# Performance work log

Measured on AMD Instinct MI355X. Metric: run time of the kernel, lower is better.

## Reference

```python
import jax, jax.numpy as jnp
import numpy as np

EPS = 1e-5

def _inst_norm(x):
    # x: (B,C,H,W); torch .var(dim=2) is unbiased (ddof=1) over HW
    B, C, H, W = x.shape
    xf = x.reshape(B, C, H * W)
    mean = xf.mean(axis=2, keepdims=True)
    var = xf.var(axis=2, ddof=1, keepdims=True) + EPS
    return ((xf - mean) / jnp.sqrt(var)).reshape(B, C, H, W)

def _conv1x1(x, w, b):
    # (out,in) weight applied channelwise
    return jnp.einsum('oc,bchw->bohw', w, x) + b[None, :, None, None]

def setup_inputs() -> dict:
    key = jax.random.key(0)
    ks = jax.random.split(key, 10)
    B, C, H, W = 4, 512, 64, 64
    s = 1.0 / np.sqrt(C)
    return {
        'x_fcc': jax.random.normal(ks[0], (B, C, H, W), jnp.float32),
        'x_fss': jax.random.normal(ks[1], (B, C, H, W), jnp.float32),
        'w1': jax.random.normal(ks[2], (C, C), jnp.float32) * s,
        'b1': jax.random.normal(ks[3], (C,), jnp.float32) * 0.01,
        'w2': jax.random.normal(ks[4], (C, C), jnp.float32) * s,
        'b2': jax.random.normal(ks[5], (C,), jnp.float32) * 0.01,
        'w3': jax.random.normal(ks[6], (C, C), jnp.float32) * s,
        'b3': jax.random.normal(ks[7], (C,), jnp.float32) * 0.01,
        'wrs': jax.random.normal(ks[8], (C, C), jnp.float32) * s,
        'brs': jax.random.normal(ks[9], (C,), jnp.float32) * 0.01,
    }

def reference(x_fcc, x_fss, w1, b1, w2, b2, w3, b3, wrs, brs):
    Bc, Cc, Hc, Wc = x_fcc.shape
    Bs, Cs, Hs, Ws = x_fss.shape
    q = _conv1x1(_inst_norm(x_fcc), w1, b1).reshape(Bc, Cc, Hc * Wc)
    k = _conv1x1(_inst_norm(x_fss), w2, b2).reshape(Bs, Cs, Hs * Ws)
    v = _conv1x1(x_fss, w3, b3).reshape(Bc, Cs, Hs * Ws)
    # attention: (B, HWc, HWs), softmax over style positions
    scores = jnp.einsum('bcq,bck->bqk', q, k)
    A = jax.nn.softmax(scores, axis=-1)
    # aggregate style values per content position: (B, C, HWc)
    frs = jnp.einsum('bck,bqk->bcq', v, A).reshape(x_fcc.shape)
    frs = _conv1x1(frs, wrs, brs)
    return frs + x_fcc
```

## Files before the change

kernel.cpp:

```cpp
#include <hip/hip_runtime.h>
#include <hip/hip_bf16.h>


typedef _Float16 f16_t;
typedef _Float16 f16x8 __attribute__((ext_vector_type(8)));
typedef float f32x4 __attribute__((ext_vector_type(4)));

#define C_DIM 512
#define HW_DIM 4096
#define NBATCH 4
#define CHW (512L * 4096L)

__device__ inline f32x4 mfma_f16(f16x8 a, f16x8 b, f32x4 c) {
    return __builtin_amdgcn_mfma_f32_16x16x32_f16(a, b, c, 0, 0, 0);
}

__device__ inline void g2l16(const f16_t* g, f16_t* l) {
    auto gp = (const __attribute__((address_space(1))) uint32_t*)(uintptr_t)g;
    auto lp = (__attribute__((address_space(3))) uint32_t*)(uint32_t)(uintptr_t)l;
    __builtin_amdgcn_global_load_lds(gp, lp, 16, 0, 0);
}

template<int N> __device__ inline void vmwait() {
    static_assert(N == 0 || N == 2, "add vmcnt case");
    if constexpr (N == 0) asm volatile("s_waitcnt vmcnt(0)" ::: "memory");
    else                  asm volatile("s_waitcnt vmcnt(2)" ::: "memory");
}

__device__ inline void barrier_mem() {
    asm volatile("s_barrier" ::: "memory");
    __builtin_amdgcn_sched_barrier(0);
}

__global__ __launch_bounds__(256) void stats_kernel(
    const float* __restrict__ xc, const float* __restrict__ xs,
    float* __restrict__ meanc, float* __restrict__ rstdc,
    float* __restrict__ means, float* __restrict__ rstds)
{
    int id = blockIdx.x;
    int bc = id & 2047;
    const float4* x = (const float4*)((id < 2048 ? xc : xs) + (size_t)bc * HW_DIM);
    int tid = threadIdx.x;
    float s = 0.f, ss = 0.f;
#pragma unroll
    for (int i = 0; i < 4; i++) {
        float4 v = x[tid + (i << 8)];
        s += v.x + v.y + v.z + v.w;
        ss += v.x * v.x + v.y * v.y + v.z * v.z + v.w * v.w;
    }
#pragma unroll
    for (int o = 32; o; o >>= 1) { s += __shfl_down(s, o); ss += __shfl_down(ss, o); }
    __shared__ float red[8];
    if ((tid & 63) == 0) { red[(tid >> 6) * 2] = s; red[(tid >> 6) * 2 + 1] = ss; }
    __syncthreads();
    if (tid == 0) {
        s  = red[0] + red[2] + red[4] + red[6];
        ss = red[1] + red[3] + red[5] + red[7];
        float mean = s * (1.0f / 4096.0f);
        float var  = (ss - 4096.0f * mean * mean) * (1.0f / 4095.0f);
        float rstd = rsqrtf(var + 1e-5f);
        if (id < 2048) { meanc[bc] = mean; rstdc[bc] = rstd; }
        else           { means[bc] = mean; rstds[bc] = rstd; }
    }
}

__global__ __launch_bounds__(256) void pack_w4_kernel(
    const float* __restrict__ w0, const float* __restrict__ w1,
    const float* __restrict__ w2, const float* __restrict__ w3,
    f16_t* __restrict__ h0, f16_t* __restrict__ h1,
    f16_t* __restrict__ h2, f16_t* __restrict__ h3,
    const float* __restrict__ bb0, const float* __restrict__ bb1,
    const float* __restrict__ bb2, const float* __restrict__ bb3,
    float* __restrict__ biasws)
{
    int which = blockIdx.y;
    const float* w = which == 0 ? w0 : which == 1 ? w1 : which == 2 ? w2 : w3;
    f16_t* h = which == 0 ? h0 : which == 1 ? h1 : which == 2 ? h2 : h3;
    const float* bs = which == 0 ? bb0 : which == 1 ? bb1 : which == 2 ? bb2 : bb3;
    int i = blockIdx.x * 256 + threadIdx.x;
    h[i] = (f16_t)w[i];
    if (i < C_DIM) biasws[which * C_DIM + i] = bs[i];
}

__global__ __launch_bounds__(256) void pack_T_kernel(
    const float* __restrict__ xc, const float* __restrict__ xs,
    const float* __restrict__ meanc, const float* __restrict__ rstdc,
    const float* __restrict__ means, const float* __restrict__ rstds,
    f16_t* __restrict__ ch, f16_t* __restrict__ sh, f16_t* __restrict__ sraw)
{
    __shared__ float tile[32][33];
    int z = blockIdx.z;
    int b = z & 3, src = z >> 2;
    const float* x    = (src == 0) ? xc : xs;
    const float* mean = (src == 0) ? meanc : means;
    const float* rstd = (src == 0) ? rstdc : rstds;

    int c0 = blockIdx.y * 32, p0 = blockIdx.x * 32;
    int tp = threadIdx.x & 31, tc8 = threadIdx.x >> 5;
    const float* xb = x + ((size_t)b * C_DIM + c0) * HW_DIM + p0;
#pragma unroll
    for (int it = 0; it < 4; it++) {
        int c = tc8 + it * 8;
        tile[c][tp] = xb[(size_t)c * HW_DIM + tp];
    }
    __syncthreads();
    int wc = threadIdx.x & 31, wp8 = threadIdx.x >> 5;
    float m = mean[b * C_DIM + c0 + wc];
    float r = rstd[b * C_DIM + c0 + wc];
    size_t obase = ((size_t)b * HW_DIM + p0) * C_DIM + c0;
    f16_t* ohb = ((src == 0) ? ch : sh) + obase;
    f16_t* srb = sraw + obase;
#pragma unroll
    for (int it = 0; it < 4; it++) {
        int p = wp8 + it * 8;
        float v = tile[wc][p];
        ohb[(size_t)p * C_DIM + wc] = (f16_t)((v - m) * r);
        if (src == 1) srb[(size_t)p * C_DIM + wc] = (f16_t)v;
    }
}

__global__ __launch_bounds__(256) void softmax_rows(
    const float* __restrict__ S, f16_t* __restrict__ P)
{
    int row = blockIdx.x;
    int tid = threadIdx.x;
    int wave = tid >> 6, lane = tid & 63;
    const float4* sr = (const float4*)(S + (size_t)row * HW_DIM);
    float4 v[4];
    float mx = -3.4e38f;
#pragma unroll
    for (int i = 0; i < 4; i++) {
        v[i] = sr[tid + (i << 8)];
        mx = fmaxf(mx, fmaxf(fmaxf(v[i].x, v[i].y), fmaxf(v[i].z, v[i].w)));
    }
#pragma unroll
    for (int o = 32; o; o >>= 1) mx = fmaxf(mx, __shfl_down(mx, o));
    __shared__ float red[4];
    if (lane == 0) red[wave] = mx;
    __syncthreads();
    mx = fmaxf(fmaxf(red[0], red[1]), fmaxf(red[2], red[3]));
    float sum = 0.f;
#pragma unroll
    for (int i = 0; i < 4; i++) {
        v[i].x = __expf(v[i].x - mx); v[i].y = __expf(v[i].y - mx);
        v[i].z = __expf(v[i].z - mx); v[i].w = __expf(v[i].w - mx);
        sum += v[i].x + v[i].y + v[i].z + v[i].w;
    }
#pragma unroll
    for (int o = 32; o; o >>= 1) sum += __shfl_down(sum, o);
    __syncthreads();
    if (lane == 0) red[wave] = sum;
    __syncthreads();
    sum = red[0] + red[1] + red[2] + red[3];
    float inv = 1.0f / sum;
    uint2* pr = (uint2*)(P + (size_t)row * HW_DIM);
#pragma unroll
    for (int i = 0; i < 4; i++) {
        union { uint2 u; f16_t h[4]; } o;
        o.h[0] = (f16_t)(v[i].x * inv); o.h[1] = (f16_t)(v[i].y * inv);
        o.h[2] = (f16_t)(v[i].z * inv); o.h[3] = (f16_t)(v[i].w * inv);
        pr[tid + (i << 8)] = o.u;
    }
}

__global__ __launch_bounds__(256) void reduce4_kernel(
    const float* __restrict__ part, f16_t* __restrict__ out)
{
    size_t i = (size_t)blockIdx.x * 256 + threadIdx.x;
    const float4* p0 = (const float4*)part;
    const float4* p1 = (const float4*)(part + CHW);
    const float4* p2 = (const float4*)(part + 2 * CHW);
    const float4* p3 = (const float4*)(part + 3 * CHW);
    float4 a = p0[i], b = p1[i], c = p2[i], d = p3[i];
    union { uint2 u; f16_t h[4]; } o;
    o.h[0] = (f16_t)(a.x + b.x + c.x + d.x);
    o.h[1] = (f16_t)(a.y + b.y + c.y + d.y);
    o.h[2] = (f16_t)(a.z + b.z + c.z + d.z);
    o.h[3] = (f16_t)(a.w + b.w + c.w + d.w);
    ((uint2*)out)[i] = o.u;
}

template<int EPI, bool QK, int NT, int CHX, int CHY>
__global__ __launch_bounds__(512, 2) void gemm256(
    const f16_t* __restrict__ Ah, const f16_t* __restrict__ Bh,
    void* __restrict__ Cout0, const float* __restrict__ bias,
    const float* __restrict__ resid,
    int lda, int ldc,
    long sAz, long sBz, long sCz, long sRz, long sAw, long sBw, long sCw)
{
    constexpr int UNIT = 128 * 64;
    __shared__ __align__(16) f16_t smem[8 * UNIT];

    int bx, by, bz;
    {
        const int nbx = gridDim.x, nby = gridDim.y, nbz = gridDim.z;
        const int lin = ((int)blockIdx.z * nby + blockIdx.y) * nbx + blockIdx.x;
        const int nwg = nbx * nby * nbz;
        const int cpx = nwg >> 3;
        const int logical = (lin & 7) * cpx + (lin >> 3);
        constexpr int CHB = CHX * CHY;
        const int chunk  = logical / CHB;
        const int within = logical % CHB;
        const int cx = within % CHX, cy = within / CHX;
        const int chunks_x = nbx / CHX;
        const int chx = chunk % chunks_x;
        int tt = chunk / chunks_x;
        const int chunks_y = nby / CHY;
        bz = tt / chunks_y;
        by = (tt % chunks_y) * CHY + cy;
        bx = chx * CHX + cx;
    }

    const int tid  = threadIdx.x;
    const int wave = tid >> 6, lane = tid & 63;
    const int wm = (wave >> 2) * 128;
    const int wn = (wave & 3) * 64;
    const int fr = lane & 15;
    const int g16 = lane >> 4;
    const int key = fr & 7;
    const int ha  = wave >> 2;
    const int hb  = wn >> 7;
    const int rB  = wn - hb * 128;

    const int z   = QK ? (bz & 3) : bz;
    const int sel = QK ? (bz >> 2) : 0;
    const f16_t* Az = Ah + (size_t)z * sAz + (size_t)sel * sAw;
    const f16_t* Bz = Bh + (size_t)z * sBz + (size_t)sel * sBw;
    const float* biasp = bias ? (bias + (QK ? sel * C_DIM : 0)) : nullptr;
    const long mBlock = (long)by * 256;
    const long nBlock = (long)bx * 256;

    const int srow8 = lane >> 3;
    const int gsrc  = ((lane & 7) ^ srow8) * 8;
    const f16_t* aRow[2][2]; const f16_t* bRow[2][2];
#pragma unroll
    for (int h = 0; h < 2; h++)
#pragma unroll
        for (int q = 0; q < 2; q++) {
            long r = q * 64 + wave * 8 + srow8;
            aRow[h][q] = Az + (size_t)(mBlock + h * 128 + r) * lda + gsrc;
            bRow[h][q] = Bz + (size_t)(nBlock + h * 128 + r) * lda + gsrc;
        }
    const int dst0 = wave * 512;
    const int dst1 = 4096 + wave * 512;

    auto stageU = [&](int t, int isB, int h) {
        f16_t* ub = smem + ((t & 1) * 4 + isB * 2 + h) * UNIT;
        const long k0 = (long)t * 64;
        if (isB) {
            g2l16(bRow[h][0] + k0, ub + dst0);
            g2l16(bRow[h][1] + k0, ub + dst1);
        } else {
            g2l16(aRow[h][0] + k0, ub + dst0);
            g2l16(aRow[h][1] + k0, ub + dst1);
        }
    };

    f32x4 acc[8][4];
#pragma unroll
    for (int i = 0; i < 8; i++)
#pragma unroll
        for (int j = 0; j < 4; j++) acc[i][j] = (f32x4){0.f, 0.f, 0.f, 0.f};

    stageU(0, 0, 0); stageU(0, 0, 1); stageU(0, 1, 0); stageU(0, 1, 1);
    if (NT > 1) stageU(1, 0, 0);
    vmwait<2>();
    barrier_mem();

#pragma unroll
    for (int t = 0; t < NT; ++t) {
        const f16_t* bufA = smem + ((t & 1) * 4 + ha) * UNIT;
        const f16_t* bufB = smem + ((t & 1) * 4 + 2 + hb) * UNIT;
#pragma unroll
        for (int ks = 0; ks < 2; ++ks) {
            const int gr = ((ks * 4 + g16) ^ key) * 8;
            f16x8 a[8], b0, b1;
#pragma unroll
            for (int mi = 0; mi < 8; mi++)
                a[mi] = *reinterpret_cast<const f16x8*>(
                    bufA + (mi * 16 + fr) * 64 + gr);
            b0 = *reinterpret_cast<const f16x8*>(bufB + (rB + fr) * 64 + gr);
            b1 = *reinterpret_cast<const f16x8*>(bufB + (rB + 16 + fr) * 64 + gr);
            if (ks == 0) { if (t + 1 < NT) stageU(t + 1, 0, 1); }
            else         { if (t + 1 < NT) stageU(t + 1, 1, 1); }
            barrier_mem();
            __builtin_amdgcn_s_setprio(1);
#pragma unroll
            for (int mi = 0; mi < 8; mi++) {
                acc[mi][0] = mfma_f16(a[mi], b0, acc[mi][0]);
                acc[mi][1] = mfma_f16(a[mi], b1, acc[mi][1]);
            }
            __builtin_amdgcn_s_setprio(0);
            barrier_mem();
            b0 = *reinterpret_cast<const f16x8*>(bufB + (rB + 32 + fr) * 64 + gr);
            b1 = *reinterpret_cast<const f16x8*>(bufB + (rB + 48 + fr) * 64 + gr);
            if (ks == 0) { if (t + 1 < NT) stageU(t + 1, 1, 0); }
            else {
                if (t + 2 < NT) { stageU(t + 2, 0, 0); vmwait<2>(); }
                else if (t + 1 < NT) vmwait<0>();
            }
            barrier_mem();
            __builtin_amdgcn_s_setprio(1);
#pragma unroll
            for (int mi = 0; mi < 8; mi++) {
                acc[mi][2] = mfma_f16(a[mi], b0, acc[mi][2]);
                acc[mi][3] = mfma_f16(a[mi], b1, acc[mi][3]);
            }
            __builtin_amdgcn_s_setprio(0);
            barrier_mem();
        }
    }

    const int col  = lane & 15;
    const int rowq = (lane >> 4) * 4;
    const size_t cbase = (size_t)z * sCz + (size_t)sel * sCw;
#pragma unroll
    for (int mi = 0; mi < 8; mi++) {
        const long mb = mBlock + wm + mi * 16 + rowq;
        float bv[4];
#pragma unroll
        for (int r = 0; r < 4; r++) bv[r] = biasp ? biasp[mb + r] : 0.0f;
#pragma unroll
        for (int j2 = 0; j2 < 4; j2++) {
            const long n = nBlock + wn + j2 * 16 + col;
            float v[4];
#pragma unroll
            for (int r = 0; r < 4; r++) v[r] = acc[mi][j2][r] + bv[r];
            if constexpr (EPI == 0) {
                float* O = (float*)Cout0 + cbase;
                const float* R = resid ? (resid + (size_t)z * sRz) : nullptr;
#pragma unroll
                for (int r = 0; r < 4; r++) {
                    size_t off = (size_t)(mb + r) * ldc + n;
                    O[off] = v[r] + (R ? R[off] : 0.0f);
                }
            } else if constexpr (EPI == 1) {
                f16_t* O = (f16_t*)Cout0 + cbase;
#pragma unroll
                for (int r = 0; r < 4; r++) O[(size_t)(mb + r) * ldc + n] = (f16_t)v[r];
            } else if constexpr (EPI == 3) {
                alignas(8) f16_t h[4];
#pragma unroll
                for (int r = 0; r < 4; r++) h[r] = (f16_t)v[r];
                *reinterpret_cast<uint2*>((f16_t*)Cout0 + cbase + (size_t)n * ldc + mb)
                    = *reinterpret_cast<uint2*>(h);
            } else {
                alignas(16) float h[4];
#pragma unroll
                for (int r = 0; r < 4; r++) h[r] = v[r];
                *reinterpret_cast<float4*>((float*)Cout0 + cbase + (size_t)n * ldc + mb)
                    = *reinterpret_cast<float4*>(h);
            }
        }
    }
}

extern "C" void kernel_launch(void* const* d_in, const int* in_sizes, int n_in,
                              void* d_out, int out_size, void* d_ws, size_t ws_size,
                              hipStream_t stream)
{
    const float* x_fcc = (const float*)d_in[0];
    const float* x_fss = (const float*)d_in[1];
    const float* w1 = (const float*)d_in[2];
    const float* b1 = (const float*)d_in[3];
    const float* w2 = (const float*)d_in[4];
    const float* b2 = (const float*)d_in[5];
    const float* w3 = (const float*)d_in[6];
    const float* b3 = (const float*)d_in[7];
    const float* wrs = (const float*)d_in[8];
    const float* brs = (const float*)d_in[9];
    float* out = (float*)d_out;
    (void)n_in; (void)in_sizes; (void)out_size; (void)ws_size;

    char* base = (char*)d_ws;
    size_t off = 0;
    auto take = [&](size_t bytes) -> char* {
        char* p = base + off;
        off += (bytes + 255) & ~(size_t)255;
        return p;
    };
    const size_t WB = (size_t)C_DIM * C_DIM * sizeof(f16_t);
    const size_t TB = (size_t)NBATCH * CHW * sizeof(f16_t);
    const long  TBe = NBATCH * CHW;

    float* meanc = (float*)take(2048 * 4);
    float* rstdc = (float*)take(2048 * 4);
    float* means = (float*)take(2048 * 4);
    float* rstds = (float*)take(2048 * 4);
    float* biasws = (float*)take(4 * C_DIM * 4);
    f16_t* w1h = (f16_t*)take(WB);
    f16_t* w2h = (f16_t*)take(WB);
    f16_t* w3h = (f16_t*)take(WB);
    f16_t* wrh = (f16_t*)take(WB);
    f16_t* qT = (f16_t*)take(TB);
    f16_t* kT = (f16_t*)take(TB);
    f16_t* vh   = (f16_t*)take(TB);
    f16_t* frsT = (f16_t*)take(TB);
    char* packb = take(8 * TB);
    f16_t* xcT  = (f16_t*)(packb);
    f16_t* xsT  = (f16_t*)(packb + TB);
    f16_t* xsrT = (f16_t*)(packb + 2 * TB);
    float* Smat = (float*)(packb);
    f16_t* Pmat = (f16_t*)(packb + 4 * TB);
    float* Part = (float*)(packb + 6 * TB);

    dim3 blk(256);
    dim3 blk5(512);

    stats_kernel<<<dim3(4096), blk, 0, stream>>>(x_fcc, x_fss, meanc, rstdc, means, rstds);
    pack_w4_kernel<<<dim3(1024, 4), blk, 0, stream>>>(
        w1, w2, w3, wrs, w1h, w2h, w3h, wrh, b1, b2, b3, brs, biasws);
    pack_T_kernel<<<dim3(128, 16, 8), blk, 0, stream>>>(
        x_fcc, x_fss, meanc, rstdc, means, rstds, xcT, xsT, xsrT);
    gemm256<3, true, 8, 8, 2><<<dim3(16, 2, 8), blk5, 0, stream>>>(
        w1h, xcT, qT, biasws, nullptr, C_DIM, C_DIM,
        0L, CHW, CHW, 0L, (long)C_DIM * C_DIM, TBe, TBe);
    gemm256<1, false, 8, 8, 2><<<dim3(16, 2, 4), blk5, 0, stream>>>(
        w3h, xsrT, vh, biasws + 2 * C_DIM, nullptr, C_DIM, HW_DIM,
        0L, CHW, CHW, 0L, 0L, 0L, 0L);
    for (int b = 0; b < NBATCH; b++) {
        gemm256<0, false, 8, 4, 8><<<dim3(16, 16, 1), blk5, 0, stream>>>(
            qT + (size_t)b * CHW, kT + (size_t)b * CHW,
            Smat, nullptr, nullptr, C_DIM, HW_DIM,
            0L, 0L, 0L, 0L, 0L, 0L, 0L);
        softmax_rows<<<dim3(4096), blk, 0, stream>>>(Smat, Pmat);
        gemm256<4, false, 16, 8, 2><<<dim3(16, 2, 4), blk5, 0, stream>>>(
            vh + (size_t)b * CHW, Pmat,
            Part, nullptr, nullptr, HW_DIM, C_DIM,
            1024L, 1024L, CHW, 0L, 0L, 0L, 0L);
        reduce4_kernel<<<dim3(CHW / 1024), blk, 0, stream>>>(
            Part, frsT + (size_t)b * CHW);
    }
    gemm256<0, false, 8, 8, 2><<<dim3(16, 2, 4), blk5, 0, stream>>>(
        wrh, frsT, out, biasws + 3 * C_DIM, x_fcc, C_DIM, HW_DIM,
        0L, CHW, CHW, CHW, 0L, 0L, 0L);
}
```

Before: 599.5 us.

## Add 256x128 triple-buffered GEMM and deepen prefetch in 256x256 GEMM

Adds a new gemm128r kernel with a 256x128 tile and a three-stage LDS ring buffer. It is used for the V projection, the P·V partial GEMMs and the output projection, which doubles their workgroup count so more CUs get work. The existing 256x256 kernel is renamed and its prefetch schedule is reordered to issue a whole K-tile ahead, with the vmcnt waits moved after the MFMAs. The triple buffer uses more LDS per block (about 144KB), which may limit occupancy, and the smaller N tile lowers data reuse per block.

```diff
diff --git a/kernel.cpp b/kernel.cpp
--- a/kernel.cpp
+++ b/kernel.cpp
@@ -22,14 +22,36 @@
 }
 
 template<int N> __device__ inline void vmwait() {
-    static_assert(N == 0 || N == 2, "add vmcnt case");
-    if constexpr (N == 0) asm volatile("s_waitcnt vmcnt(0)" ::: "memory");
-    else                  asm volatile("s_waitcnt vmcnt(2)" ::: "memory");
+    static_assert(N == 0 || N == 2 || N == 4 || N == 6, "add vmcnt case");
+    if constexpr (N == 0)      asm volatile("s_waitcnt vmcnt(0)" ::: "memory");
+    else if constexpr (N == 2) asm volatile("s_waitcnt vmcnt(2)" ::: "memory");
+    else if constexpr (N == 4) asm volatile("s_waitcnt vmcnt(4)" ::: "memory");
+    else                       asm volatile("s_waitcnt vmcnt(6)" ::: "memory");
 }
 
 __device__ inline void barrier_mem() {
     asm volatile("s_barrier" ::: "memory");
     __builtin_amdgcn_sched_barrier(0);
+}
+
+template<int CHX, int CHY>
+__device__ inline void xcd_swizzle(int& bx, int& by, int& bz) {
+    const int nbx = gridDim.x, nby = gridDim.y, nbz = gridDim.z;
+    const int lin = ((int)blockIdx.z * nby + blockIdx.y) * nbx + blockIdx.x;
+    const int nwg = nbx * nby * nbz;
+    const int cpx = nwg >> 3;
+    const int logical = (lin & 7) * cpx + (lin >> 3);
+    constexpr int CHB = CHX * CHY;
+    const int chunk  = logical / CHB;
+    const int within = logical % CHB;
+    const int cx = within % CHX, cy = within / CHX;
+    const int chunks_x = nbx / CHX;
+    const int chx = chunk % chunks_x;
+    int tt = chunk / chunks_x;
+    const int chunks_y = nby / CHY;
+    bz = tt / chunks_y;
+    by = (tt % chunks_y) * CHY + cy;
+    bx = chx * CHX + cx;
 }
 
 __global__ __launch_bounds__(256) void stats_kernel(
@@ -181,7 +203,7 @@
 }
 
 template<int EPI, bool QK, int NT, int CHX, int CHY>
-__global__ __launch_bounds__(512, 2) void gemm256(
+__global__ __launch_bounds__(512, 2) void gemm256d(
     const f16_t* __restrict__ Ah, const f16_t* __restrict__ Bh,
     void* __restrict__ Cout0, const float* __restrict__ bias,
     const float* __restrict__ resid,
@@ -192,24 +214,7 @@
     __shared__ __align__(16) f16_t smem[8 * UNIT];
 
     int bx, by, bz;
-    {
-        const int nbx = gridDim.x, nby = gridDim.y, nbz = gridDim.z;
-        const int lin = ((int)blockIdx.z * nby + blockIdx.y) * nbx + blockIdx.x;
-        const int nwg = nbx * nby * nbz;
-        const int cpx = nwg >> 3;
-        const int logical = (lin & 7) * cpx + (lin >> 3);
-        constexpr int CHB = CHX * CHY;
-        const int chunk  = logical / CHB;
-        const int within = logical % CHB;
-        const int cx = within % CHX, cy = within / CHX;
-        const int chunks_x = nbx / CHX;
-        const int chx = chunk % chunks_x;
-        int tt = chunk / chunks_x;
-        const int chunks_y = nby / CHY;
-        bz = tt / chunks_y;
-        by = (tt % chunks_y) * CHY + cy;
-        bx = chx * CHX + cx;
-    }
+    xcd_swizzle<CHX, CHY>(bx, by, bz);
 
     const int tid  = threadIdx.x;
     const int wave = tid >> 6, lane = tid & 63;
@@ -263,8 +268,8 @@
         for (int j = 0; j < 4; j++) acc[i][j] = (f32x4){0.f, 0.f, 0.f, 0.f};
 
     stageU(0, 0, 0); stageU(0, 0, 1); stageU(0, 1, 0); stageU(0, 1, 1);
-    if (NT > 1) stageU(1, 0, 0);
-    vmwait<2>();
+    if (NT > 1) { stageU(1, 0, 0); stageU(1, 0, 1); }
+    vmwait<4>();
     barrier_mem();
 
 #pragma unroll
@@ -281,8 +286,7 @@
                     bufA + (mi * 16 + fr) * 64 + gr);
             b0 = *reinterpret_cast<const f16x8*>(bufB + (rB + fr) * 64 + gr);
             b1 = *reinterpret_cast<const f16x8*>(bufB + (rB + 16 + fr) * 64 + gr);
-            if (ks == 0) { if (t + 1 < NT) stageU(t + 1, 0, 1); }
-            else         { if (t + 1 < NT) stageU(t + 1, 1, 1); }
+            if (ks == 0 && t + 1 < NT) stageU(t + 1, 1, 0);
             barrier_mem();
             __builtin_amdgcn_s_setprio(1);
 #pragma unroll
@@ -294,10 +298,10 @@
             barrier_mem();
             b0 = *reinterpret_cast<const f16x8*>(bufB + (rB + 32 + fr) * 64 + gr);
             b1 = *reinterpret_cast<const f16x8*>(bufB + (rB + 48 + fr) * 64 + gr);
-            if (ks == 0) { if (t + 1 < NT) stageU(t + 1, 1, 0); }
-            else {
-                if (t + 2 < NT) { stageU(t + 2, 0, 0); vmwait<2>(); }
-                else if (t + 1 < NT) vmwait<0>();
+            if (ks == 0) {
+                if (t + 1 < NT) stageU(t + 1, 1, 1);
+            } else {
+                if (t + 2 < NT) { stageU(t + 2, 0, 0); stageU(t + 2, 0, 1); }
             }
             barrier_mem();
             __builtin_amdgcn_s_setprio(1);
@@ -307,6 +311,10 @@
                 acc[mi][3] = mfma_f16(a[mi], b1, acc[mi][3]);
             }
             __builtin_amdgcn_s_setprio(0);
+            if (ks == 1) {
+                if (t + 2 < NT)      vmwait<4>();
+                else if (t + 1 < NT) vmwait<0>();
+            }
             barrier_mem();
         }
     }
@@ -322,6 +330,152 @@
         for (int r = 0; r < 4; r++) bv[r] = biasp ? biasp[mb + r] : 0.0f;
 #pragma unroll
         for (int j2 = 0; j2 < 4; j2++) {
+            const long n = nBlock + wn + j2 * 16 + col;
+            float v[4];
+#pragma unroll
+            for (int r = 0; r < 4; r++) v[r] = acc[mi][j2][r] + bv[r];
+            if constexpr (EPI == 0) {
+                float* O = (float*)Cout0 + cbase;
+                const float* R = resid ? (resid + (size_t)z * sRz) : nullptr;
+#pragma unroll
+                for (int r = 0; r < 4; r++) {
+                    size_t off = (size_t)(mb + r) * ldc + n;
+                    O[off] = v[r] + (R ? R[off] : 0.0f);
+                }
+            } else if constexpr (EPI == 1) {
+                f16_t* O = (f16_t*)Cout0 + cbase;
+#pragma unroll
+                for (int r = 0; r < 4; r++) O[(size_t)(mb + r) * ldc + n] = (f16_t)v[r];
+            } else if constexpr (EPI == 3) {
+                alignas(8) f16_t h[4];
+#pragma unroll
+                for (int r = 0; r < 4; r++) h[r] = (f16_t)v[r];
+                *reinterpret_cast<uint2*>((f16_t*)Cout0 + cbase + (size_t)n * ldc + mb)
+                    = *reinterpret_cast<uint2*>(h);
+            } else {
+                alignas(16) float h[4];
+#pragma unroll
+                for (int r = 0; r < 4; r++) h[r] = v[r];
+                *reinterpret_cast<float4*>((float*)Cout0 + cbase + (size_t)n * ldc + mb)
+                    = *reinterpret_cast<float4*>(h);
+            }
+        }
+    }
+}
+
+template<int EPI, bool QK, int NT, int CHX, int CHY>
+__global__ __launch_bounds__(512, 2) void gemm128r(
+    const f16_t* __restrict__ Ah, const f16_t* __restrict__ Bh,
+    void* __restrict__ Cout0, const float* __restrict__ bias,
+    const float* __restrict__ resid,
+    int lda, int ldc,
+    long sAz, long sBz, long sCz, long sRz, long sAw, long sBw, long sCw)
+{
+    constexpr int AE = 256 * 64;
+    constexpr int BE = 128 * 64;
+    constexpr int BUFE = AE + BE;
+    __shared__ __align__(16) f16_t smem[3 * BUFE];
+
+    int bx, by, bz;
+    xcd_swizzle<CHX, CHY>(bx, by, bz);
+
+    const int tid  = threadIdx.x;
+    const int wave = tid >> 6, lane = tid & 63;
+    const int wm = (wave >> 2) * 128;
+    const int wn = (wave & 3) * 32;
+    const int fr = lane & 15;
+    const int g16 = lane >> 4;
+    const int key = fr & 7;
+
+    const int z   = QK ? (bz & 3) : bz;
+    const int sel = QK ? (bz >> 2) : 0;
+    const f16_t* Az = Ah + (size_t)z * sAz + (size_t)sel * sAw;
+    const f16_t* Bz = Bh + (size_t)z * sBz + (size_t)sel * sBw;
+    const float* biasp = bias ? (bias + (QK ? sel * C_DIM : 0)) : nullptr;
+    const long mBlock = (long)by * 256;
+    const long nBlock = (long)bx * 128;
+
+    const int srow8 = lane >> 3;
+    const int gsrc  = ((lane & 7) ^ srow8) * 8;
+    const f16_t* aSrc[4]; const f16_t* bSrc[2];
+    int aDst[4], bDst[2];
+#pragma unroll
+    for (int q = 0; q < 4; q++) {
+        int j = 4 * wave + q;
+        aSrc[q] = Az + (size_t)(mBlock + 8 * j + srow8) * lda + gsrc;
+        aDst[q] = j * 512;
+    }
+#pragma unroll
+    for (int q = 0; q < 2; q++) {
+        int j = 2 * wave + q;
+        bSrc[q] = Bz + (size_t)(nBlock + 8 * j + srow8) * lda + gsrc;
+        bDst[q] = AE + j * 512;
+    }
+
+    auto stageA = [&](int t) {
+        f16_t* dst = smem + (t % 3) * BUFE;
+        const int k0 = t * 64;
+#pragma unroll
+        for (int q = 0; q < 4; q++) g2l16(aSrc[q] + k0, dst + aDst[q]);
+    };
+    auto stageB = [&](int t) {
+        f16_t* dst = smem + (t % 3) * BUFE;
+        const int k0 = t * 64;
+#pragma unroll
+        for (int q = 0; q < 2; q++) g2l16(bSrc[q] + k0, dst + bDst[q]);
+    };
+
+    f32x4 acc[8][2];
+#pragma unroll
+    for (int i = 0; i < 8; i++)
+#pragma unroll
+        for (int j = 0; j < 2; j++) acc[i][j] = (f32x4){0.f, 0.f, 0.f, 0.f};
+
+    stageA(0); stageB(0); stageA(1); stageB(1);
+    vmwait<6>();
+    barrier_mem();
+
+#pragma unroll
+    for (int t = 0; t < NT; ++t) {
+        const f16_t* buf = smem + (t % 3) * BUFE;
+#pragma unroll
+        for (int ks = 0; ks < 2; ++ks) {
+            f16x8 a[8], b0, b1;
+            const int gr = ((ks * 4 + g16) ^ key) * 8;
+#pragma unroll
+            for (int mi = 0; mi < 8; mi++)
+                a[mi] = *reinterpret_cast<const f16x8*>(
+                    buf + (wm + mi * 16 + fr) * 64 + gr);
+            b0 = *reinterpret_cast<const f16x8*>(buf + AE + (wn + fr) * 64 + gr);
+            b1 = *reinterpret_cast<const f16x8*>(buf + AE + (wn + 16 + fr) * 64 + gr);
+            if (t + 2 < NT) { if (ks == 0) stageA(t + 2); else stageB(t + 2); }
+            if (ks == 1) {
+                if (t + 2 < NT)      vmwait<6>();
+                else if (t + 1 < NT) vmwait<0>();
+            }
+            barrier_mem();
+            __builtin_amdgcn_s_setprio(1);
+#pragma unroll
+            for (int mi = 0; mi < 8; mi++) {
+                acc[mi][0] = mfma_f16(a[mi], b0, acc[mi][0]);
+                acc[mi][1] = mfma_f16(a[mi], b1, acc[mi][1]);
+            }
+            __builtin_amdgcn_s_setprio(0);
+            barrier_mem();
+        }
+    }
+
+    const int col  = lane & 15;
+    const int rowq = (lane >> 4) * 4;
+    const size_t cbase = (size_t)z * sCz + (size_t)sel * sCw;
+#pragma unroll
+    for (int mi = 0; mi < 8; mi++) {
+        const long mb = mBlock + wm + mi * 16 + rowq;
+        float bv[4];
+#pragma unroll
+        for (int r = 0; r < 4; r++) bv[r] = biasp ? biasp[mb + r] : 0.0f;
+#pragma unroll
+        for (int j2 = 0; j2 < 2; j2++) {
             const long n = nBlock + wn + j2 * 16 + col;
             float v[4];
 #pragma unroll
@@ -412,26 +566,26 @@
         w1, w2, w3, wrs, w1h, w2h, w3h, wrh, b1, b2, b3, brs, biasws);
     pack_T_kernel<<<dim3(128, 16, 8), blk, 0, stream>>>(
         x_fcc, x_fss, meanc, rstdc, means, rstds, xcT, xsT, xsrT);
-    gemm256<3, true, 8, 8, 2><<<dim3(16, 2, 8), blk5, 0, stream>>>(
+    gemm256d<3, true, 8, 8, 2><<<dim3(16, 2, 8), blk5, 0, stream>>>(
         w1h, xcT, qT, biasws, nullptr, C_DIM, C_DIM,
         0L, CHW, CHW, 0L, (long)C_DIM * C_DIM, TBe, TBe);
-    gemm256<1, false, 8, 8, 2><<<dim3(16, 2, 4), blk5, 0, stream>>>(
+    gemm128r<1, false, 8, 8, 2><<<dim3(32, 2, 4), blk5, 0, stream>>>(
         w3h, xsrT, vh, biasws + 2 * C_DIM, nullptr, C_DIM, HW_DIM,
         0L, CHW, CHW, 0L, 0L, 0L, 0L);
     for (int b = 0; b < NBATCH; b++) {
-        gemm256<0, false, 8, 4, 8><<<dim3(16, 16, 1), blk5, 0, stream>>>(
+        gemm256d<0, false, 8, 4, 8><<<dim3(16, 16, 1), blk5, 0, stream>>>(
             qT + (size_t)b * CHW, kT + (size_t)b * CHW,
             Smat, nullptr, nullptr, C_DIM, HW_DIM,
             0L, 0L, 0L, 0L, 0L, 0L, 0L);
         softmax_rows<<<dim3(4096), blk, 0, stream>>>(Smat, Pmat);
-        gemm256<4, false, 16, 8, 2><<<dim3(16, 2, 4), blk5, 0, stream>>>(
+        gemm128r<4, false, 16, 8, 2><<<dim3(32, 2, 4), blk5, 0, stream>>>(
             vh + (size_t)b * CHW, Pmat,
             Part, nullptr, nullptr, HW_DIM, C_DIM,
             1024L, 1024L, CHW, 0L, 0L, 0L, 0L);
         reduce4_kernel<<<dim3(CHW / 1024), blk, 0, stream>>>(
             Part, frsT + (size_t)b * CHW);
     }
-    gemm256<0, false, 8, 8, 2><<<dim3(16, 2, 4), blk5, 0, stream>>>(
+    gemm128r<0, false, 8, 8, 2><<<dim3(32, 2, 4), blk5, 0, stream>>>(
         wrh, frsT, out, biasws + 3 * C_DIM, x_fcc, C_DIM, HW_DIM,
         0L, CHW, CHW, CHW, 0L, 0L, 0L);
 }
```

Result: faster. 521.1 us (-13.1%).
